# Kernel tuning notes

Measured on AMD Instinct MI355X. Metric: run time of the kernel, lower is better.

Reference implementation:

```python
import jax, jax.numpy as jnp
import numpy as np

EPS = 1e-6
WEIGHTS = dict(segmentation=1.0, absence=2.0, attention_supervision=0.3,
               confidence=0.1, dice=1.0, false_positive_suppression=0.5)


def setup_inputs() -> dict:
    key = jax.random.key(0)
    ks = jax.random.split(key, 6)
    B, S, H, W = 8, 12, 512, 512
    seg_logits = jax.random.normal(ks[0], (B, S, H, W), dtype=jnp.float32)
    seg_probs = jax.nn.sigmoid(jax.random.normal(ks[1], (B, S, H, W), dtype=jnp.float32))
    seg_targets = (jax.random.uniform(ks[2], (B, S, H, W)) < 0.3).astype(jnp.float32)
    presence_probs = jnp.clip(jax.random.uniform(ks[3], (B, S)), 1e-6, 1.0 - 1e-6)
    presence_targets = (jax.random.uniform(ks[4], (B, S)) < 0.7).astype(jnp.float32)
    attention_maps = jnp.clip(jax.random.uniform(ks[5], (B, S, H, W)), 1e-6, 1.0 - 1e-6)
    return {"seg_logits": seg_logits, "seg_probs": seg_probs,
            "presence_probs": presence_probs, "attention_maps": attention_maps,
            "seg_targets": seg_targets, "presence_targets": presence_targets}


def _bce(p, t):
    # torch BCELoss: -(t*log(p) + (1-t)*log(1-p)), logs clamped to >= -100
    return -(t * jnp.clip(jnp.log(p), -100.0, None)
             + (1.0 - t) * jnp.clip(jnp.log1p(-p), -100.0, None))


def _bce_with_logits(x, t):
    # stable: max(x,0) - x*t + log(1+exp(-|x|))
    return jnp.maximum(x, 0.0) - x * t + jnp.log1p(jnp.exp(-jnp.abs(x)))


def reference(seg_logits, seg_probs, presence_probs, attention_maps,
              seg_targets, presence_targets):
    B, S = presence_targets.shape
    mask = presence_targets != 0          # [B,S] present structures
    maskf = mask.astype(seg_logits.dtype)
    n_valid = maskf.sum()
    n_absent = (1.0 - maskf).sum()

    # per-(b,s) segmentation BCE (mean over spatial)
    seg_bce_bs = _bce_with_logits(seg_logits, seg_targets).mean(axis=(-2, -1))  # [B,S]
    # per-(b,s) dice loss (each original call is on a [1,1,...] slice)
    inter = jnp.sum(seg_probs * seg_targets, axis=(-2, -1))
    psum = jnp.sum(seg_probs, axis=(-2, -1))
    tsum = jnp.sum(seg_targets, axis=(-2, -1))
    dice_bs = 1.0 - (2.0 * inter + EPS) / (psum + tsum + EPS)                   # [B,S]

    seg_loss = jnp.where(n_valid > 0, jnp.sum(seg_bce_bs * maskf) / jnp.maximum(n_valid, 1.0), 0.0)
    dice_loss = jnp.where(n_valid > 0, jnp.sum(dice_bs * maskf) / jnp.maximum(n_valid, 1.0), 0.0)

    # false positive suppression on absent structures
    fp_bs = jnp.maximum(seg_probs, 0.0).mean(axis=(-2, -1))                     # [B,S]
    fp_loss = jnp.where(n_absent > 0,
                        jnp.sum(fp_bs * (1.0 - maskf)) / jnp.maximum(n_absent, 1.0), 0.0)

    # presence/absence BCE over all (b,s)
    absence_loss = _bce(presence_probs, presence_targets).mean()

    # attention supervision on present structures, normalized by B*S
    att_target = (seg_targets > 0.5).astype(seg_targets.dtype)
    att_bce_bs = _bce(attention_maps, att_target).mean(axis=(-2, -1))           # [B,S]
    att_loss = jnp.sum(att_bce_bs * maskf) / (B * S)

    # confidence calibration penalty
    p, t = presence_probs, presence_targets
    conf = (jnp.where((t == 0) & (p > 0.5), (p - 0.5) ** 2, 0.0)
            + jnp.where((t == 1) & (p < 0.5), (0.5 - p) ** 2, 0.0))
    conf_loss = conf.sum() / (B * S)

    total = (WEIGHTS['segmentation'] * seg_loss + WEIGHTS['dice'] * dice_loss
             + WEIGHTS['absence'] * absence_loss
             + WEIGHTS['attention_supervision'] * att_loss
             + WEIGHTS['confidence'] * conf_loss
             + WEIGHTS['false_positive_suppression'] * fp_loss)

    return jnp.stack([total, seg_loss, dice_loss, absence_loss,
                      att_loss, conf_loss, fp_loss])
```

## Files before the change

### kernel.cpp

```cpp
#include <hip/hip_runtime.h>
#include <hip/hip_bf16.h>


constexpr int kB = 8, kS = 12, kH = 512, kW = 512;
constexpr int kSlices = kB * kS;
constexpr long kHW = (long)kH * kW;
constexpr int kVecPerSlice = (int)(kHW / 4);
constexpr int kBlocksPerSlice = 32;
constexpr int kBlock = 256;
constexpr int kVecPerBlock = kVecPerSlice / kBlocksPerSlice;
constexpr int kIters = kVecPerBlock / kBlock;
constexpr float kEPS = 1e-6f;


__global__ __launch_bounds__(kBlock) void slice_reduce_kernel(
    const float4* __restrict__ logits,
    const float4* __restrict__ probs,
    const float4* __restrict__ att,
    const float4* __restrict__ tgt,
    float* __restrict__ partial) {
  const int gid = blockIdx.x;
  const int slice = gid >> 5;
  const int chunk = gid & (kBlocksPerSlice - 1);
  const long base = (long)slice * kVecPerSlice + (long)chunk * kVecPerBlock
                    + threadIdx.x;

  float s_bce = 0.f, s_inter = 0.f, s_p = 0.f, s_t = 0.f, s_fp = 0.f,
        s_att = 0.f;

#pragma unroll
  for (int k = 0; k < kIters; ++k) {
    const long idx = base + (long)k * kBlock;
    const float4 x4 = logits[idx];
    const float4 p4 = probs[idx];
    const float4 a4 = att[idx];
    const float4 t4 = tgt[idx];
    const float xs[4] = {x4.x, x4.y, x4.z, x4.w};
    const float ps[4] = {p4.x, p4.y, p4.z, p4.w};
    const float as[4] = {a4.x, a4.y, a4.z, a4.w};
    const float ts[4] = {t4.x, t4.y, t4.z, t4.w};
#pragma unroll
    for (int j = 0; j < 4; ++j) {
      const float x = xs[j], p = ps[j], a = as[j], t = ts[j];
      s_bce += fmaxf(x, 0.f) - x * t + log1pf(expf(-fabsf(x)));
      s_inter += p * t;
      s_p += p;
      s_t += t;
      s_fp += fmaxf(p, 0.f);
      const float la = fmaxf(logf(a), -100.f);
      const float l1a = fmaxf(log1pf(-a), -100.f);
      s_att += (t > 0.5f) ? -la : -l1a;
    }
  }

  float vals[6] = {s_bce, s_inter, s_p, s_t, s_fp, s_att};
  const int lane = threadIdx.x & 63;
  const int wave = threadIdx.x >> 6;
  __shared__ float lds[4][6];
#pragma unroll
  for (int q = 0; q < 6; ++q) {
    float v = vals[q];
    for (int off = 32; off > 0; off >>= 1) v += __shfl_down(v, off, 64);
    if (lane == 0) lds[wave][q] = v;
  }
  __syncthreads();
  if (threadIdx.x == 0) {
#pragma unroll
    for (int q = 0; q < 6; ++q) {
      const float v = lds[0][q] + lds[1][q] + lds[2][q] + lds[3][q];
      atomicAdd(&partial[slice * 6 + q], v);
    }
  }
}

__global__ __launch_bounds__(128) void finalize_kernel(
    const float* __restrict__ partial,
    const float* __restrict__ pprobs,
    const float* __restrict__ ptgt,
    float* __restrict__ out) {
  const int i = threadIdx.x;
  __shared__ float acc[7][128];
  float q[7] = {0.f, 0.f, 0.f, 0.f, 0.f, 0.f, 0.f};
  if (i < kSlices) {
    const float t = ptgt[i];
    const float m = (t != 0.f) ? 1.f : 0.f;
    const float inv = 1.f / (float)kHW;
    const float bce = partial[i * 6 + 0] * inv;
    const float inter = partial[i * 6 + 1];
    const float psum = partial[i * 6 + 2];
    const float tsum = partial[i * 6 + 3];
    const float fp = partial[i * 6 + 4] * inv;
    const float att = partial[i * 6 + 5] * inv;
    const float dice = 1.f - (2.f * inter + kEPS) / (psum + tsum + kEPS);
    q[0] = bce * m;
    q[1] = dice * m;
    q[2] = fp * (1.f - m);
    q[3] = att * m;
    const float p = pprobs[i];
    q[4] = -(t * fmaxf(logf(p), -100.f) +
             (1.f - t) * fmaxf(log1pf(-p), -100.f));
    float c = 0.f;
    if (t == 0.f && p > 0.5f) c += (p - 0.5f) * (p - 0.5f);
    if (t == 1.f && p < 0.5f) c += (0.5f - p) * (0.5f - p);
    q[5] = c;
    q[6] = m;
  }
#pragma unroll
  for (int k = 0; k < 7; ++k) acc[k][i] = q[k];
  __syncthreads();
  if (i == 0) {
    float s[7];
#pragma unroll
    for (int k = 0; k < 7; ++k) {
      float v = 0.f;
      for (int j = 0; j < kSlices; ++j) v += acc[k][j];
      s[k] = v;
    }
    const float n_valid = s[6];
    const float n_absent = (float)kSlices - n_valid;
    const float seg_loss = (n_valid > 0.f) ? s[0] / fmaxf(n_valid, 1.f) : 0.f;
    const float dice_loss = (n_valid > 0.f) ? s[1] / fmaxf(n_valid, 1.f) : 0.f;
    const float fp_loss = (n_absent > 0.f) ? s[2] / fmaxf(n_absent, 1.f) : 0.f;
    const float att_loss = s[3] / (float)kSlices;
    const float absence_loss = s[4] / (float)kSlices;
    const float conf_loss = s[5] / (float)kSlices;
    const float total = 1.0f * seg_loss + 1.0f * dice_loss +
                        2.0f * absence_loss + 0.3f * att_loss +
                        0.1f * conf_loss + 0.5f * fp_loss;
    out[0] = total;
    out[1] = seg_loss;
    out[2] = dice_loss;
    out[3] = absence_loss;
    out[4] = att_loss;
    out[5] = conf_loss;
    out[6] = fp_loss;
  }
}

extern "C" void kernel_launch(void* const* d_in, const int* in_sizes, int n_in,
                              void* d_out, int out_size, void* d_ws,
                              size_t ws_size, hipStream_t stream) {
  const float4* seg_logits = (const float4*)d_in[0];
  const float4* seg_probs = (const float4*)d_in[1];
  const float* presence_probs = (const float*)d_in[2];
  const float4* attention_maps = (const float4*)d_in[3];
  const float4* seg_targets = (const float4*)d_in[4];
  const float* presence_targets = (const float*)d_in[5];
  float* out = (float*)d_out;
  float* partial = (float*)d_ws;

  hipMemsetAsync(partial, 0, kSlices * 6 * sizeof(float), stream);

  slice_reduce_kernel<<<kSlices * kBlocksPerSlice, kBlock, 0, stream>>>(
      seg_logits, seg_probs, attention_maps, seg_targets, partial);
  finalize_kernel<<<1, 128, 0, stream>>>(partial, presence_probs,
                                         presence_targets, out);
}
```

Before: 380.3 us.

## Use hardware exp2/log intrinsics and quadruple blocks per slice

Replaces the libm expf/log1pf/logf calls with the AMD hardware exp2 and log2 builtins, scaling by log2(e) and ln2. The attention BCE now takes a single log of the selected value (a or 1-a) instead of computing both logs. It also raises the block count per slice from 32 to 128, so each thread handles two float4 vectors loaded up front rather than looping over eight. The aim is to cut transcendental ALU cost and give more blocks to hide memory latency. In exchange it loses the -100 clamp and log1p accuracy, and quadruples the atomic adds into the partial buffer.

```diff
diff --git a/kernel.cpp b/kernel.cpp
--- a/kernel.cpp
+++ b/kernel.cpp
@@ -6,11 +6,12 @@
 constexpr int kSlices = kB * kS;
 constexpr long kHW = (long)kH * kW;
 constexpr int kVecPerSlice = (int)(kHW / 4);
-constexpr int kBlocksPerSlice = 32;
+constexpr int kBlocksPerSlice = 128;
 constexpr int kBlock = 256;
 constexpr int kVecPerBlock = kVecPerSlice / kBlocksPerSlice;
-constexpr int kIters = kVecPerBlock / kBlock;
 constexpr float kEPS = 1e-6f;
+constexpr float kLOG2E = 1.44269504088896340736f;
+constexpr float kLN2 = 0.69314718055994530942f;
 
 
 __global__ __launch_bounds__(kBlock) void slice_reduce_kernel(
@@ -20,37 +21,39 @@
     const float4* __restrict__ tgt,
     float* __restrict__ partial) {
   const int gid = blockIdx.x;
-  const int slice = gid >> 5;
+  const int slice = gid >> 7;
   const int chunk = gid & (kBlocksPerSlice - 1);
   const long base = (long)slice * kVecPerSlice + (long)chunk * kVecPerBlock
                     + threadIdx.x;
 
+  const float4 x0 = logits[base];
+  const float4 x1 = logits[base + kBlock];
+  const float4 p0 = probs[base];
+  const float4 p1 = probs[base + kBlock];
+  const float4 a0 = att[base];
+  const float4 a1 = att[base + kBlock];
+  const float4 t0 = tgt[base];
+  const float4 t1 = tgt[base + kBlock];
+
   float s_bce = 0.f, s_inter = 0.f, s_p = 0.f, s_t = 0.f, s_fp = 0.f,
         s_att = 0.f;
 
+  const float xs[8] = {x0.x, x0.y, x0.z, x0.w, x1.x, x1.y, x1.z, x1.w};
+  const float ps[8] = {p0.x, p0.y, p0.z, p0.w, p1.x, p1.y, p1.z, p1.w};
+  const float as[8] = {a0.x, a0.y, a0.z, a0.w, a1.x, a1.y, a1.z, a1.w};
+  const float ts[8] = {t0.x, t0.y, t0.z, t0.w, t1.x, t1.y, t1.z, t1.w};
+
 #pragma unroll
-  for (int k = 0; k < kIters; ++k) {
-    const long idx = base + (long)k * kBlock;
-    const float4 x4 = logits[idx];
-    const float4 p4 = probs[idx];
-    const float4 a4 = att[idx];
-    const float4 t4 = tgt[idx];
-    const float xs[4] = {x4.x, x4.y, x4.z, x4.w};
-    const float ps[4] = {p4.x, p4.y, p4.z, p4.w};
-    const float as[4] = {a4.x, a4.y, a4.z, a4.w};
-    const float ts[4] = {t4.x, t4.y, t4.z, t4.w};
-#pragma unroll
-    for (int j = 0; j < 4; ++j) {
-      const float x = xs[j], p = ps[j], a = as[j], t = ts[j];
-      s_bce += fmaxf(x, 0.f) - x * t + log1pf(expf(-fabsf(x)));
-      s_inter += p * t;
-      s_p += p;
-      s_t += t;
-      s_fp += fmaxf(p, 0.f);
-      const float la = fmaxf(logf(a), -100.f);
-      const float l1a = fmaxf(log1pf(-a), -100.f);
-      s_att += (t > 0.5f) ? -la : -l1a;
-    }
+  for (int j = 0; j < 8; ++j) {
+    const float x = xs[j], p = ps[j], a = as[j], t = ts[j];
+    const float u = __builtin_amdgcn_exp2f(-fabsf(x) * kLOG2E);
+    s_bce += fmaxf(x, 0.f) - x * t + kLN2 * __builtin_amdgcn_logf(1.f + u);
+    s_inter += p * t;
+    s_p += p;
+    s_t += t;
+    s_fp += fmaxf(p, 0.f);
+    const float c = (t > 0.5f) ? a : 1.0f - a;
+    s_att -= kLN2 * __builtin_amdgcn_logf(c);
   }
 
   float vals[6] = {s_bce, s_inter, s_p, s_t, s_fp, s_att};
@@ -90,12 +93,12 @@
     const float psum = partial[i * 6 + 2];
     const float tsum = partial[i * 6 + 3];
     const float fp = partial[i * 6 + 4] * inv;
-    const float att = partial[i * 6 + 5] * inv;
+    const float attv = partial[i * 6 + 5] * inv;
     const float dice = 1.f - (2.f * inter + kEPS) / (psum + tsum + kEPS);
     q[0] = bce * m;
     q[1] = dice * m;
     q[2] = fp * (1.f - m);
-    q[3] = att * m;
+    q[3] = attv * m;
     const float p = pprobs[i];
     q[4] = -(t * fmaxf(logf(p), -100.f) +
              (1.f - t) * fmaxf(log1pf(-p), -100.f));
```

Result: slower. 401.5 us (+5.6%).
